# Optimization experiments

Measured on AMD Instinct MI355X. Metric: run time of the kernel, lower is better.

Reference implementation:

```python
import jax, jax.numpy as jnp
import numpy as np

B, N, PAST = 2, 1024, 1024
DIM, HEADS, DH = 2048, 16, 128
INNER = HEADS * DH
LN_EPS = 1e-5
ROPE_THETA = 10000.0


def setup_inputs() -> dict:
    key = jax.random.key(0)
    k0, k1, k2, k3, k4 = jax.random.split(key, 5)
    x = jax.random.normal(k0, (B, N, DIM), dtype=jnp.float32)
    past_k = jax.random.normal(k1, (B, HEADS, PAST, DH), dtype=jnp.float32)
    past_v = jax.random.normal(k2, (B, HEADS, PAST, DH), dtype=jnp.float32)
    # causal mask with KV-cache offset: query i sits at global pos PAST+i,
    # mask (True = blocked) keys at positions j > PAST+i
    kv = PAST + N
    q_pos = PAST + jnp.arange(N)
    k_pos = jnp.arange(kv)
    mask = jnp.broadcast_to((k_pos[None, :] > q_pos[:, None])[None, None], (B, 1, N, kv))
    w_qkv = jax.random.normal(k3, (DIM, 3 * INNER), dtype=jnp.float32) * (DIM ** -0.5)
    w_out = jax.random.normal(k4, (INNER, DIM), dtype=jnp.float32) * (INNER ** -0.5)
    ln_g = jnp.ones((DIM,), dtype=jnp.float32)
    ln_b = jnp.zeros((DIM,), dtype=jnp.float32)
    return {"x": x, "past_k": past_k, "past_v": past_v, "mask": mask,
            "w_qkv": w_qkv, "w_out": w_out, "ln_g": ln_g, "ln_b": ln_b}


def _layernorm(x, g, b):
    mu = jnp.mean(x, axis=-1, keepdims=True)
    var = jnp.mean((x - mu) ** 2, axis=-1, keepdims=True)
    return (x - mu) * jax.lax.rsqrt(var + LN_EPS) * g + b


def _rope(t, pos):
    # interleaved rotary (lucidrains rotary-embedding-torch convention)
    inv_freq = 1.0 / (ROPE_THETA ** (jnp.arange(0, DH, 2, dtype=jnp.float32) / DH))
    freqs = pos.astype(jnp.float32)[:, None] * inv_freq[None, :]   # [n, DH/2]
    freqs = jnp.repeat(freqs, 2, axis=-1)                          # [n, DH]
    cos = jnp.cos(freqs).astype(t.dtype)
    sin = jnp.sin(freqs).astype(t.dtype)
    t2 = t.reshape(*t.shape[:-1], DH // 2, 2)
    rot = jnp.stack((-t2[..., 1], t2[..., 0]), axis=-1).reshape(t.shape)
    return t * cos + rot * sin


def reference(x, past_k, past_v, mask, w_qkv, w_out, ln_g, ln_b):
    b, n, _ = x.shape
    xn = _layernorm(x, ln_g, ln_b)
    qkv = xn @ w_qkv                                               # [b, n, 3*INNER]
    q, k, v = jnp.split(qkv, 3, axis=-1)
    to_heads = lambda t: t.reshape(b, n, HEADS, DH).transpose(0, 2, 1, 3)  # b h n d
    q, k, v = to_heads(q), to_heads(k), to_heads(v)
    k = jnp.concatenate((past_k, k), axis=2)                       # [b, h, kv, d]
    v = jnp.concatenate((past_v, v), axis=2)
    kv_len = k.shape[2]
    q = _rope(q, jnp.arange(n) + (kv_len - n))
    k = _rope(k, jnp.arange(kv_len))
    scale = DH ** -0.5
    dots = jnp.einsum('bhnd,bhmd->bhnm', q, k) * scale             # [b, h, n, kv]
    dots = jnp.where(mask, -jnp.inf, dots)
    attn = jax.nn.softmax(dots, axis=-1)
    out = jnp.einsum('bhnm,bhmd->bhnd', attn, v)                   # [b, h, n, d]
    out = out.transpose(0, 2, 1, 3).reshape(b, n, INNER)
    return out @ w_out, k, v
```

## Files before the change

kernel.cpp:

```cpp
#include <hip/hip_runtime.h>
#include <hip/hip_bf16.h>
#include <math.h>

#define BB    2
#define NN    1024
#define PAST  1024
#define KVL   2048
#define DIM   2048
#define HEADS 16
#define DH    128
#define INNER 2048
#define NQKV  6144
#define TOK   2048
#define LN_EPS 1e-5f

typedef __attribute__((ext_vector_type(8)))  short    short8;
typedef __attribute__((ext_vector_type(4)))  float    f32x4;
typedef __attribute__((ext_vector_type(16))) float    f32x16;
typedef __attribute__((ext_vector_type(8)))  unsigned short us8;
typedef __attribute__((ext_vector_type(4)))  unsigned short us4;
typedef unsigned short us;

__device__ __forceinline__ float bfbits2f(us u) {
    return __uint_as_float(((unsigned int)u) << 16);
}
__device__ __forceinline__ us f2bfb(float f) {
    union { __hip_bfloat16 h; us u; } cv;
    cv.h = __float2bfloat16(f);
    return cv.u;
}
__device__ __forceinline__ unsigned pkbf(float a, float b) {
    return (unsigned)f2bfb(a) | ((unsigned)f2bfb(b) << 16);
}
__device__ __forceinline__ us8 pack8u(float4 a, float4 b) {
    us8 r;
    r[0] = f2bfb(a.x); r[1] = f2bfb(a.y); r[2] = f2bfb(a.z); r[3] = f2bfb(a.w);
    r[4] = f2bfb(b.x); r[5] = f2bfb(b.y); r[6] = f2bfb(b.z); r[7] = f2bfb(b.w);
    return r;
}

__device__ __forceinline__ void gload_lds16(const void* gsrc, void* ldst) {
    __builtin_amdgcn_global_load_lds(
        (const __attribute__((address_space(1))) void*)gsrc,
        (__attribute__((address_space(3))) void*)ldst, 16, 0, 0);
}

__global__ __launch_bounds__(256) void transp_kernel(
    const float* __restrict__ src, us* __restrict__ dst, int R, int C)
{
    const int c0 = blockIdx.x * 64;
    const int r0 = blockIdx.y * 64;
    const int tid = threadIdx.x;

    __shared__ us T[64][68];

    #pragma unroll
    for (int e = 0; e < 4; e++) {
        int idx = tid + e * 256;
        int jr  = idx >> 4;
        int c4  = (idx & 15) * 4;
        float4 v = *reinterpret_cast<const float4*>(
            src + (size_t)(r0 + jr) * C + c0 + c4);
        us4 w;
        w[0] = f2bfb(v.x); w[1] = f2bfb(v.y); w[2] = f2bfb(v.z); w[3] = f2bfb(v.w);
        *reinterpret_cast<us4*>(&T[jr][c4]) = w;
    }
    __syncthreads();

    #pragma unroll
    for (int e = 0; e < 4; e++) {
        int idx = tid + e * 256;
        int d   = idx >> 4;
        int k4  = (idx & 15) * 4;
        us4 w;
        w[0] = T[k4 + 0][d];
        w[1] = T[k4 + 1][d];
        w[2] = T[k4 + 2][d];
        w[3] = T[k4 + 3][d];
        *reinterpret_cast<us4*>(dst + (size_t)(c0 + d) * R + r0 + k4) = w;
    }
}

__global__ __launch_bounds__(256) void ln_kernel(
    const float* __restrict__ x, const float* __restrict__ g,
    const float* __restrict__ b, us* __restrict__ xn)
{
    const int t   = blockIdx.x;
    const int tid = threadIdx.x;
    const size_t base = (size_t)t * DIM;

    float4 p0 = reinterpret_cast<const float4*>(x + base)[tid * 2 + 0];
    float4 p1 = reinterpret_cast<const float4*>(x + base)[tid * 2 + 1];
    float v[8] = {p0.x, p0.y, p0.z, p0.w, p1.x, p1.y, p1.z, p1.w};

    float s1 = 0.f, s2 = 0.f;
    #pragma unroll
    for (int i = 0; i < 8; i++) { s1 += v[i]; s2 += v[i] * v[i]; }

    #pragma unroll
    for (int off = 32; off; off >>= 1) {
        s1 += __shfl_xor(s1, off);
        s2 += __shfl_xor(s2, off);
    }
    __shared__ float red1[4], red2[4];
    if ((tid & 63) == 0) { red1[tid >> 6] = s1; red2[tid >> 6] = s2; }
    __syncthreads();
    float S1 = red1[0] + red1[1] + red1[2] + red1[3];
    float S2 = red2[0] + red2[1] + red2[2] + red2[3];
    const float inv = 1.0f / (float)DIM;
    float mu  = S1 * inv;
    float var = S2 * inv - mu * mu;
    float rstd = rsqrtf(var + LN_EPS);

    const int d0 = tid * 8;
    float4 oa, ob;
    oa.x = (v[0] - mu) * rstd * g[d0 + 0] + b[d0 + 0];
    oa.y = (v[1] - mu) * rstd * g[d0 + 1] + b[d0 + 1];
    oa.z = (v[2] - mu) * rstd * g[d0 + 2] + b[d0 + 2];
    oa.w = (v[3] - mu) * rstd * g[d0 + 3] + b[d0 + 3];
    ob.x = (v[4] - mu) * rstd * g[d0 + 4] + b[d0 + 4];
    ob.y = (v[5] - mu) * rstd * g[d0 + 5] + b[d0 + 5];
    ob.z = (v[6] - mu) * rstd * g[d0 + 6] + b[d0 + 6];
    ob.w = (v[7] - mu) * rstd * g[d0 + 7] + b[d0 + 7];

    *reinterpret_cast<us8*>(xn + base + d0) = pack8u(oa, ob);
}

template<bool OUT_BF16>
__global__ __launch_bounds__(256) void gemm_bt_kernel(
    const us* __restrict__ A, const us* __restrict__ Bt,
    void* __restrict__ Cout, int M, int N, int K)
{
    __shared__ us As[3][128 * 32];
    __shared__ us Bs[3][128 * 32];

    const int tid  = threadIdx.x;
    const int wave = tid >> 6, lane = tid & 63;
    const int quad = lane >> 4, l16 = lane & 15;
    const int wm = wave & 1, wn = wave >> 1;
    const int m0 = blockIdx.y * 128, n0 = blockIdx.x * 128;

    f32x4 acc[4][4];
    #pragma unroll
    for (int i = 0; i < 4; i++)
        #pragma unroll
        for (int j = 0; j < 4; j++)
            #pragma unroll
            for (int r = 0; r < 4; r++) acc[i][j][r] = 0.f;

    auto stage = [&](int k0, int buf) {
        #pragma unroll
        for (int e = 0; e < 2; e++) {
            int phys = (e * 256 + tid) * 16;
            int lr   = phys >> 7;
            int offp = (phys & 127) ^ ((lr & 7) << 4);
            int m    = 2 * lr + (offp >> 6);
            int kb   = offp & 63;
            gload_lds16((const char*)(A + (size_t)(m0 + m) * K + k0) + kb,
                        (char*)&As[buf][0] + phys);
            gload_lds16((const char*)(Bt + (size_t)(n0 + m) * K + k0) + kb,
                        (char*)&Bs[buf][0] + phys);
        }
    };

    const int ns = K >> 5;
    stage(0, 0);
    stage(32, 1);
    __builtin_amdgcn_sched_barrier(0);
    asm volatile("s_waitcnt vmcnt(4)" ::: "memory");
    __builtin_amdgcn_s_barrier();
    __builtin_amdgcn_sched_barrier(0);

    int cur = 0;
    for (int ks = 0; ks < ns; ks++) {
        if (ks + 2 < ns) stage((ks + 2) * 32, (ks + 2) % 3);

        short8 af[4], bf[4];
        #pragma unroll
        for (int mi = 0; mi < 4; mi++) {
            int mrow = wm * 64 + mi * 16 + l16;
            int lr   = mrow >> 1;
            int off  = ((mrow & 1) * 64 + quad * 16) ^ ((lr & 7) << 4);
            af[mi] = *reinterpret_cast<const short8*>(
                (const char*)&As[cur][0] + lr * 128 + off);
        }
        #pragma unroll
        for (int ni = 0; ni < 4; ni++) {
            int nrow = wn * 64 + ni * 16 + l16;
            int lr   = nrow >> 1;
            int off  = ((nrow & 1) * 64 + quad * 16) ^ ((lr & 7) << 4);
            bf[ni] = *reinterpret_cast<const short8*>(
                (const char*)&Bs[cur][0] + lr * 128 + off);
        }

        __builtin_amdgcn_s_setprio(1);
        #pragma unroll
        for (int mi = 0; mi < 4; mi++)
            #pragma unroll
            for (int ni = 0; ni < 4; ni++)
                acc[mi][ni] = __builtin_amdgcn_mfma_f32_16x16x32_bf16(
                    af[mi], bf[ni], acc[mi][ni], 0, 0, 0);
        __builtin_amdgcn_s_setprio(0);

        __builtin_amdgcn_sched_barrier(0);
        if (ks + 2 < ns) asm volatile("s_waitcnt vmcnt(4)" ::: "memory");
        else             asm volatile("s_waitcnt vmcnt(0)" ::: "memory");
        __builtin_amdgcn_s_barrier();
        __builtin_amdgcn_sched_barrier(0);
        cur = (cur == 2) ? 0 : cur + 1;
    }

    #pragma unroll
    for (int mi = 0; mi < 4; mi++) {
        #pragma unroll
        for (int r = 0; r < 4; r++) {
            size_t row = (size_t)(m0 + wm * 64 + mi * 16 + quad * 4 + r);
            #pragma unroll
            for (int ni = 0; ni < 4; ni++) {
                size_t col = n0 + wn * 64 + ni * 16 + l16;
                if (OUT_BF16)
                    ((us*)Cout)[row * N + col] = f2bfb(acc[mi][ni][r]);
                else
                    ((float*)Cout)[row * N + col] = acc[mi][ni][r];
            }
        }
    }
}

__global__ __launch_bounds__(256) void rope_kernel(
    const float* __restrict__ past_k, const float* __restrict__ past_v,
    us* __restrict__ qkv, float* __restrict__ out_k, float* __restrict__ out_v,
    us* __restrict__ Kbf)
{
    const int tid  = threadIdx.x;
    const int pid  = blockIdx.x * 4 + (tid >> 6);
    const int lane = tid & 63;

    const int b   = pid / (HEADS * KVL);
    const int rem = pid - b * (HEADS * KVL);
    const int h   = rem / KVL;
    const int pos = rem - h * KVL;

    const float invf = exp2f((float)lane * (-13.287712379549449f / 64.0f));
    float sn, cs;
    sincosf((float)pos * invf, &sn, &cs);

    const size_t obase = ((size_t)(b * HEADS + h) * KVL + pos) * DH + 2 * lane;

    float k0, k1;
    if (pos < PAST) {
        const size_t pbase = ((size_t)(b * HEADS + h) * PAST + pos) * DH + 2 * lane;
        k0 = past_k[pbase];
        k1 = past_k[pbase + 1];
    } else {
        const int t = b * NN + (pos - PAST);
        const us* qp = qkv + (size_t)t * NQKV + INNER + h * DH + 2 * lane;
        k0 = bfbits2f(qp[0]); k1 = bfbits2f(qp[1]);
    }
    float kr0 = k0 * cs - k1 * sn;
    float kr1 = k1 * cs + k0 * sn;
    out_k[obase]     = kr0;
    out_k[obase + 1] = kr1;
    Kbf[obase]       = f2bfb(kr0);
    Kbf[obase + 1]   = f2bfb(kr1);

    if (pos < PAST) {
        const size_t pbase = ((size_t)(b * HEADS + h) * PAST + pos) * DH + 2 * lane;
        out_v[obase]     = past_v[pbase];
        out_v[obase + 1] = past_v[pbase + 1];
    } else {
        const int t = b * NN + (pos - PAST);
        const us* vp = qkv + (size_t)t * NQKV + 2 * INNER + h * DH + 2 * lane;
        out_v[obase]     = bfbits2f(vp[0]);
        out_v[obase + 1] = bfbits2f(vp[1]);
    }

    if (pos >= PAST) {
        const int t = b * NN + (pos - PAST);
        us* qq = qkv + (size_t)t * NQKV + h * DH + 2 * lane;
        float q0 = bfbits2f(qq[0]), q1 = bfbits2f(qq[1]);
        qq[0] = f2bfb(q0 * cs - q1 * sn);
        qq[1] = f2bfb(q1 * cs + q0 * sn);
    }
}

__global__ __launch_bounds__(256) void vtrans_kernel(
    const float* __restrict__ Vc, us* __restrict__ Vtg)
{
    const int jb = blockIdx.x;
    const int db = blockIdx.y;
    const int bh = blockIdx.z;
    const int tid = threadIdx.x;

    __shared__ us T[64][68];

    const float* src = Vc + ((size_t)bh * KVL + jb * 64) * DH + db * 64;
    #pragma unroll
    for (int e = 0; e < 4; e++) {
        int idx = tid + e * 256;
        int jr  = idx >> 4;
        int c4  = (idx & 15) * 4;
        float4 v = *reinterpret_cast<const float4*>(src + (size_t)jr * DH + c4);
        us4 w;
        w[0] = f2bfb(v.x); w[1] = f2bfb(v.y); w[2] = f2bfb(v.z); w[3] = f2bfb(v.w);
        *reinterpret_cast<us4*>(&T[jr][c4]) = w;
    }
    __syncthreads();

    us* dst = Vtg + ((size_t)bh * DH + db * 64) * KVL + jb * 64;
    #pragma unroll
    for (int e = 0; e < 4; e++) {
        int idx = tid + e * 256;
        int d   = idx >> 4;
        int k4  = (idx & 15) * 4;
        us4 w;
        w[0] = T[k4 + 0][d];
        w[1] = T[k4 + 1][d];
        w[2] = T[k4 + 2][d];
        w[3] = T[k4 + 3][d];
        *reinterpret_cast<us4*>(dst + (size_t)d * KVL + k4) = w;
    }
}

__global__ __launch_bounds__(256) void attn_mfma_kernel(
    const us* __restrict__ qkv,
    const us* __restrict__ Kbf,
    const us* __restrict__ Vtg,
    us* __restrict__ Ao)
{
    const int tid  = threadIdx.x;
    const int wave = tid >> 6;
    const int lane = tid & 63;
    const int l32  = lane & 31;
    const int g    = lane >> 5;

    const int flat = blockIdx.x;
    const int s    = flat >> 3;
    const int grp  = (flat & 7) + 8 * (s & 3);
    const int p    = s >> 2;
    const int h    = grp & 15;
    const int b    = grp >> 4;
    const int qtile = (wave < 2) ? p : (15 - p);
    const int qsub  = (wave & 1) * 32;
    const int mynch = 17 + qtile;
    const int nch   = 32 - p;

    __shared__ us Ks[2][64 * 128];
    __shared__ us Vt[2][64 * 128];

    short8 qf[8];
    {
        const int qrow = qtile * 64 + qsub + l32;
        const us* qp = qkv + (size_t)(b * NN + qrow) * NQKV + h * DH;
        #pragma unroll
        for (int ks = 0; ks < 8; ks++)
            qf[ks] = *reinterpret_cast<const short8*>(qp + ks * 16 + g * 8);
    }

    f32x16 Oacc[4];
    #pragma unroll
    for (int dt = 0; dt < 4; dt++)
        #pragma unroll
        for (int r = 0; r < 16; r++) Oacc[dt][r] = 0.f;
    float m_run  = -INFINITY;
    float l_part = 0.f;

    const us* kptr = Kbf + (size_t)(b * HEADS + h) * KVL * DH;
    const us* vtb  = Vtg + (size_t)(b * HEADS + h) * DH * KVL;
    const float scale = 0.08838834764831845f;
    const float THRU  = 90.50966799f;
    const int qgmin = PAST + qtile * 64 + qsub;
    const int qg    = qgmin + l32;

    auto stage = [&](int j0, int buf) {
        #pragma unroll
        for (int e = 0; e < 4; e++) {
            int phys = (e * 256 + tid) * 16;
            int row  = phys >> 8;
            int col  = (phys & 255) ^ ((row & 15) << 4);
            gload_lds16((const char*)(kptr + (size_t)(j0 + row) * DH) + col,
                        (char*)&Ks[buf][0] + phys);
        }
        #pragma unroll
        for (int e = 0; e < 4; e++) {
            int phys = (e * 256 + tid) * 16;
            int row  = phys >> 8;
            int offp = (phys & 255) ^ ((row & 15) << 4);
            int d    = row + 64 * (offp >> 7);
            int cb   = offp & 127;
            gload_lds16((const char*)(vtb + (size_t)d * KVL) + j0 * 2 + cb,
                        (char*)&Vt[buf][0] + phys);
        }
    };

    stage(0, 0);
    asm volatile("s_waitcnt vmcnt(0)" ::: "memory");
    __builtin_amdgcn_s_barrier();
    __builtin_amdgcn_sched_barrier(0);

    int cur = 0;
    for (int c = 0; c < nch; c++) {
        const int j0 = c * 64;
        if (c + 1 < nch) stage(j0 + 64, cur ^ 1);

        if (c < mynch) {
            f32x16 S[2];
            #pragma unroll
            for (int t = 0; t < 2; t++)
                #pragma unroll
                for (int r = 0; r < 16; r++) S[t][r] = 0.f;

            __builtin_amdgcn_s_setprio(1);
            #pragma unroll
            for (int ks = 0; ks < 8; ks++) {
                #pragma unroll
                for (int t = 0; t < 2; t++) {
                    int row  = t * 32 + l32;
                    int colb = ks * 32 + g * 16;
                    const char* kp = (const char*)&Ks[cur][0] +
                                     row * 256 + (colb ^ ((row & 15) << 4));
                    short8 kb = *reinterpret_cast<const short8*>(kp);
                    S[t] = __builtin_amdgcn_mfma_f32_32x32x16_bf16(
                        kb, qf[ks], S[t], 0, 0, 0);
                }
            }
            __builtin_amdgcn_s_setprio(0);

            if (j0 + 63 > qgmin) {
                const int rel = qg - j0;
                #pragma unroll
                for (int t = 0; t < 2; t++)
                    #pragma unroll
                    for (int r = 0; r < 16; r++) {
                        int kvo = t * 32 + (r & 3) + 8 * (r >> 2) + 4 * g;
                        S[t][r] = (kvo <= rel) ? S[t][r] : -INFINITY;
                    }
            }
            float mx = -INFINITY;
            #pragma unroll
            for (int t = 0; t < 2; t++)
                #pragma unroll
                for (int r = 0; r < 16; r++) mx = fmaxf(mx, S[t][r]);
            mx = fmaxf(mx, __shfl_xor(mx, 32));

            float alpha = 1.f;
            if (__any(mx > m_run + THRU)) {
                float nm = fmaxf(m_run, mx);
                alpha = __expf((m_run - nm) * scale);
                m_run = nm;
                #pragma unroll
                for (int r = 0; r < 16; r++) {
                    float ar = __shfl(alpha, (r & 3) + 8 * (r >> 2) + 4 * g);
                    Oacc[0][r] *= ar; Oacc[1][r] *= ar;
                    Oacc[2][r] *= ar; Oacc[3][r] *= ar;
                }
            }

            const float nmk = -m_run * scale;
            float rs = 0.f;
            #pragma unroll
            for (int t = 0; t < 2; t++)
                #pragma unroll
                for (int r = 0; r < 16; r++) {
                    float pv = __expf(fmaf(S[t][r], scale, nmk));
                    S[t][r] = pv;
                    rs += pv;
                }
            l_part = l_part * alpha + rs;

            short8 paf[4];
            #pragma unroll
            for (int t = 0; t < 2; t++)
                #pragma unroll
                for (int u = 0; u < 2; u++) {
                    unsigned cA = pkbf(S[t][8*u + 0], S[t][8*u + 1]);
                    unsigned cB = pkbf(S[t][8*u + 2], S[t][8*u + 3]);
                    unsigned dA = pkbf(S[t][8*u + 4], S[t][8*u + 5]);
                    unsigned dB = pkbf(S[t][8*u + 6], S[t][8*u + 7]);
                    asm volatile("v_permlane32_swap_b32 %0, %1"
                                 : "+v"(cA), "+v"(dA));
                    asm volatile("v_permlane32_swap_b32 %0, %1"
                                 : "+v"(cB), "+v"(dB));
                    union { unsigned u4[4]; short8 s8; } fb;
                    fb.u4[0] = cA; fb.u4[1] = cB; fb.u4[2] = dA; fb.u4[3] = dB;
                    paf[t * 2 + u] = fb.s8;
                }

            __builtin_amdgcn_s_setprio(1);
            #pragma unroll
            for (int ks = 0; ks < 4; ks++) {
                #pragma unroll
                for (int dt = 0; dt < 4; dt++) {
                    int d    = dt * 32 + l32;
                    int lr   = d & 63;
                    int off  = (((d >> 6) << 7) + ks * 32 + g * 16)
                               ^ ((lr & 15) << 4);
                    const char* vp = (const char*)&Vt[cur][0] +
                                     lr * 256 + off;
                    short8 vb = *reinterpret_cast<const short8*>(vp);
                    Oacc[dt] = __builtin_amdgcn_mfma_f32_32x32x16_bf16(
                        paf[ks], vb, Oacc[dt], 0, 0, 0);
                }
            }
            __builtin_amdgcn_s_setprio(0);
        }

        __builtin_amdgcn_sched_barrier(0);
        asm volatile("s_waitcnt vmcnt(0)" ::: "memory");
        __builtin_amdgcn_s_barrier();
        __builtin_amdgcn_sched_barrier(0);
        cur ^= 1;
    }

    l_part += __shfl_xor(l_part, 32);
    float linv = 1.f / l_part;
    #pragma unroll
    for (int r = 0; r < 16; r++) {
        int qr = (r & 3) + 8 * (r >> 2) + 4 * g;
        float iv = __shfl(linv, qr);
        int qrow = qtile * 64 + qsub + qr;
        us* dst = Ao + (size_t)(b * NN + qrow) * INNER + h * DH + l32;
        #pragma unroll
        for (int dt = 0; dt < 4; dt++)
            dst[dt * 32] = f2bfb(Oacc[dt][r] * iv);
    }
}

extern "C" void kernel_launch(void* const* d_in, const int* in_sizes, int n_in,
                              void* d_out, int out_size, void* d_ws, size_t ws_size,
                              hipStream_t stream)
{
    const float* x      = (const float*)d_in[0];
    const float* past_k = (const float*)d_in[1];
    const float* past_v = (const float*)d_in[2];
    const float* w_qkv  = (const float*)d_in[4];
    const float* w_out  = (const float*)d_in[5];
    const float* ln_g   = (const float*)d_in[6];
    const float* ln_b   = (const float*)d_in[7];

    float* out   = (float*)d_out;
    float* out_k = out   + (size_t)BB * NN * DIM;
    float* out_v = out_k + (size_t)BB * HEADS * KVL * DH;

    us* xn   = (us*)d_ws;
    us* qkv  = xn  + (size_t)TOK * DIM;
    us* Wqt  = qkv + (size_t)TOK * NQKV;
    us* Wot  = Wqt + (size_t)NQKV * DIM;
    us* Vtg  = Wot + (size_t)DIM * INNER;
    us* attn = xn;
    us* Kbf  = Wqt;

    transp_kernel<<<dim3(NQKV / 64, DIM / 64), 256, 0, stream>>>(
        w_qkv, Wqt, DIM, NQKV);
    transp_kernel<<<dim3(DIM / 64, INNER / 64), 256, 0, stream>>>(
        w_out, Wot, INNER, DIM);

    ln_kernel<<<TOK, 256, 0, stream>>>(x, ln_g, ln_b, xn);

    gemm_bt_kernel<true><<<dim3(NQKV / 128, TOK / 128), 256, 0, stream>>>(
        xn, Wqt, (void*)qkv, TOK, NQKV, DIM);

    rope_kernel<<<(BB * HEADS * KVL) / 4, 256, 0, stream>>>(
        past_k, past_v, qkv, out_k, out_v, Kbf);

    vtrans_kernel<<<dim3(KVL / 64, DH / 64, BB * HEADS), 256, 0, stream>>>(
        out_v, Vtg);

    attn_mfma_kernel<<<256, 256, 0, stream>>>(
        qkv, Kbf, Vtg, attn);

    gemm_bt_kernel<false><<<dim3(DIM / 128, TOK / 128), 256, 0, stream>>>(
        attn, Wot, (void*)out, TOK, DIM, INNER);
}
```

Before: 388.4 us.

## Split attention KV chunks across two wave groups with LDS merge of partial softmax

Doubles the attention block to 512 threads. Each group of four waves processes alternating 64-key chunks, so two chunks are staged per iteration into doubled LDS buffers. At the end the odd group writes its running max, sum and O accumulators to LDS, and the even group merges them flash-decoding style before writing the output. This is meant to raise parallelism and hide latency with only 256 blocks on the device, at the cost of double the LDS use, extra register pressure under the new launch bound, and a final LDS merge step.

```diff
diff --git a/kernel.cpp b/kernel.cpp
--- a/kernel.cpp
+++ b/kernel.cpp
@@ -322,7 +322,7 @@
     }
 }
 
-__global__ __launch_bounds__(256) void attn_mfma_kernel(
+__global__ __launch_bounds__(512) void attn_mfma_kernel(
     const us* __restrict__ qkv,
     const us* __restrict__ Kbf,
     const us* __restrict__ Vtg,
@@ -333,6 +333,8 @@
     const int lane = tid & 63;
     const int l32  = lane & 31;
     const int g    = lane >> 5;
+    const int wv   = wave & 3;
+    const int mypar= wave >> 2;
 
     const int flat = blockIdx.x;
     const int s    = flat >> 3;
@@ -340,13 +342,14 @@
     const int p    = s >> 2;
     const int h    = grp & 15;
     const int b    = grp >> 4;
-    const int qtile = (wave < 2) ? p : (15 - p);
-    const int qsub  = (wave & 1) * 32;
+    const int qtile = (wv < 2) ? p : (15 - p);
+    const int qsub  = (wv & 1) * 32;
     const int mynch = 17 + qtile;
     const int nch   = 32 - p;
-
-    __shared__ us Ks[2][64 * 128];
-    __shared__ us Vt[2][64 * 128];
+    const int nit   = (nch + 1) >> 1;
+
+    __shared__ us Ks[2][2 * 64 * 128];
+    __shared__ us Vt[2][2 * 64 * 128];
 
     short8 qf[8];
     {
@@ -372,22 +375,28 @@
     const int qgmin = PAST + qtile * 64 + qsub;
     const int qg    = qgmin + l32;
 
-    auto stage = [&](int j0, int buf) {
+    auto stage = [&](int it2, int buf) {
         #pragma unroll
         for (int e = 0; e < 4; e++) {
-            int phys = (e * 256 + tid) * 16;
-            int row  = phys >> 8;
-            int col  = (phys & 255) ^ ((row & 15) << 4);
+            int phys = (e * 512 + tid) * 16;
+            int par  = phys >> 14;
+            int pc   = phys & 16383;
+            int row  = pc >> 8;
+            int col  = (pc & 255) ^ ((row & 15) << 4);
+            int j0   = (2 * it2 + par) * 64;
             gload_lds16((const char*)(kptr + (size_t)(j0 + row) * DH) + col,
                         (char*)&Ks[buf][0] + phys);
         }
         #pragma unroll
         for (int e = 0; e < 4; e++) {
-            int phys = (e * 256 + tid) * 16;
-            int row  = phys >> 8;
-            int offp = (phys & 255) ^ ((row & 15) << 4);
+            int phys = (e * 512 + tid) * 16;
+            int par  = phys >> 14;
+            int pc   = phys & 16383;
+            int row  = pc >> 8;
+            int offp = (pc & 255) ^ ((row & 15) << 4);
             int d    = row + 64 * (offp >> 7);
             int cb   = offp & 127;
+            int j0   = (2 * it2 + par) * 64;
             gload_lds16((const char*)(vtb + (size_t)d * KVL) + j0 * 2 + cb,
                         (char*)&Vt[buf][0] + phys);
         }
@@ -399,11 +408,15 @@
     __builtin_amdgcn_sched_barrier(0);
 
     int cur = 0;
-    for (int c = 0; c < nch; c++) {
-        const int j0 = c * 64;
-        if (c + 1 < nch) stage(j0 + 64, cur ^ 1);
-
+    for (int it = 0; it < nit; it++) {
+        if (it + 1 < nit) stage(it + 1, cur ^ 1);
+
+        const int c = 2 * it + mypar;
         if (c < mynch) {
+            const int j0 = c * 64;
+            const char* kbase = (const char*)&Ks[cur][0] + mypar * 16384;
+            const char* vbase = (const char*)&Vt[cur][0] + mypar * 16384;
+
             f32x16 S[2];
             #pragma unroll
             for (int t = 0; t < 2; t++)
@@ -417,7 +430,7 @@
                 for (int t = 0; t < 2; t++) {
                     int row  = t * 32 + l32;
                     int colb = ks * 32 + g * 16;
-                    const char* kp = (const char*)&Ks[cur][0] +
+                    const char* kp = kbase +
                                      row * 256 + (colb ^ ((row & 15) << 4));
                     short8 kb = *reinterpret_cast<const short8*>(kp);
                     S[t] = __builtin_amdgcn_mfma_f32_32x32x16_bf16(
@@ -495,8 +508,7 @@
                     int lr   = d & 63;
                     int off  = (((d >> 6) << 7) + ks * 32 + g * 16)
                                ^ ((lr & 15) << 4);
-                    const char* vp = (const char*)&Vt[cur][0] +
-                                     lr * 256 + off;
+                    const char* vp = vbase + lr * 256 + off;
                     short8 vb = *reinterpret_cast<const short8*>(vp);
                     Oacc[dt] = __builtin_amdgcn_mfma_f32_32x32x16_bf16(
                         paf[ks], vb, Oacc[dt], 0, 0, 0);
@@ -513,16 +525,46 @@
     }
 
     l_part += __shfl_xor(l_part, 32);
-    float linv = 1.f / l_part;
-    #pragma unroll
-    for (int r = 0; r < 16; r++) {
-        int qr = (r & 3) + 8 * (r >> 2) + 4 * g;
-        float iv = __shfl(linv, qr);
-        int qrow = qtile * 64 + qsub + qr;
-        us* dst = Ao + (size_t)(b * NN + qrow) * INNER + h * DH + l32;
+
+    float* scr = (float*)&Ks[0][0];
+    float* Sm  = scr;
+    float* Sl  = scr + 256;
+    float* SO  = scr + 512;
+
+    if (mypar == 1) {
+        Sm[wv * 64 + lane] = m_run;
+        Sl[wv * 64 + lane] = l_part;
+        float* ob = SO + wv * 4096 + lane;
         #pragma unroll
         for (int dt = 0; dt < 4; dt++)
-            dst[dt * 32] = f2bfb(Oacc[dt][r] * iv);
+            #pragma unroll
+            for (int r = 0; r < 16; r++)
+                ob[(dt * 16 + r) * 64] = Oacc[dt][r];
+    }
+    __syncthreads();
+    if (mypar == 0) {
+        float m1 = Sm[wv * 64 + lane];
+        float l1 = Sl[wv * 64 + lane];
+        float M  = fmaxf(m_run, m1);
+        float f0 = __expf((m_run - M) * scale);
+        float f1 = __expf((m1 - M) * scale);
+        float linv = 1.f / (l_part * f0 + l1 * f1);
+
+        const float* ob = SO + wv * 4096 + lane;
+        #pragma unroll
+        for (int r = 0; r < 16; r++) {
+            int qr = (r & 3) + 8 * (r >> 2) + 4 * g;
+            float ivr = __shfl(linv, qr);
+            float f0r = __shfl(f0, qr);
+            float f1r = __shfl(f1, qr);
+            int qrow = qtile * 64 + qsub + qr;
+            us* dst = Ao + (size_t)(b * NN + qrow) * INNER + h * DH + l32;
+            #pragma unroll
+            for (int dt = 0; dt < 4; dt++) {
+                float o1 = ob[(dt * 16 + r) * 64];
+                dst[dt * 32] = f2bfb((Oacc[dt][r] * f0r + o1 * f1r) * ivr);
+            }
+        }
     }
 }
 
@@ -566,7 +608,7 @@
     vtrans_kernel<<<dim3(KVL / 64, DH / 64, BB * HEADS), 256, 0, stream>>>(
         out_v, Vtg);
 
-    attn_mfma_kernel<<<256, 256, 0, stream>>>(
+    attn_mfma_kernel<<<256, 512, 0, stream>>>(
         qkv, Kbf, Vtg, attn);
 
     gemm_bt_kernel<false><<<dim3(DIM / 128, TOK / 128), 256, 0, stream>>>(
```

New measurement: 362.9 us. -6.5%, faster.
